# Kernel tuning notes

Hardware: AMD Instinct MI355X
Metric: run time of the kernel (lower is better)

## Reference

```python
import jax, jax.numpy as jnp
import numpy as np

NUM_NODES = 100000
FEAT_DIM = 256
H1 = 256
H2 = 256
NUM_CLASSES = 64
B = 4096
F1 = 25
F2 = 10


def setup_inputs() -> dict:
    key = jax.random.key(0)
    k0, k1, k2, ke, kw1, kw2, kw3 = jax.random.split(key, 7)
    T0 = jax.random.randint(k0, (B,), 0, NUM_NODES)
    T1 = jax.random.randint(k1, (B, F1), 0, NUM_NODES)
    T2 = jax.random.randint(k2, (B * F1, F2), 0, NUM_NODES)
    emb = jax.random.normal(ke, (NUM_NODES, FEAT_DIM), dtype=jnp.float32)
    # nn.Linear(in, out, bias=False) stores weight as [out, in]
    W1 = jax.random.normal(kw1, (H1, 2 * FEAT_DIM), dtype=jnp.float32) * (1.0 / np.sqrt(2 * FEAT_DIM))
    W2 = jax.random.normal(kw2, (H2, 2 * H1), dtype=jnp.float32) * (1.0 / np.sqrt(2 * H1))
    W3 = jax.random.normal(kw3, (NUM_CLASSES, H2), dtype=jnp.float32) * (1.0 / np.sqrt(H2))
    return {"T0": T0, "T1": T1, "T2": T2, "emb": emb, "W1": W1, "W2": W2, "W3": W3}


def reference(T0, T1, T2, emb, W1, W2, W3):
    # hop-0 roots: [B, D]; hop-1 neighbor mean: [B, D]
    feat_0 = emb[T0]
    x = emb[T1].mean(axis=1)
    h0 = jax.nn.relu(jnp.concatenate([feat_0, x], axis=1) @ W1.T)  # [B, H1]
    # dropout is identity in eval mode (p applied only in training)
    # hop-1 nodes with hop-2 neighbor mean: [B*F1, D] each
    feat_1 = emb[T1].reshape(-1, FEAT_DIM)
    x2 = emb[T2].mean(axis=1)  # [B*F1, D]
    h1 = jax.nn.relu(jnp.concatenate([feat_1, x2], axis=1) @ W1.T)  # [B*F1, H1]
    h1 = h1.reshape(B, F1, H1).mean(axis=1)  # [B, H1]
    combined = jnp.concatenate([h0, h1], axis=1)  # [B, 2*H1]
    embedding = jax.nn.relu(combined @ W2.T)  # [B, H2]
    scores = embedding @ W3.T  # [B, C]
    return scores
```

## Files before the change

kernel.cpp:

```cpp
#include <hip/hip_runtime.h>
#include <hip/hip_bf16.h>


typedef __bf16  bf16x8 __attribute__((ext_vector_type(8)));
typedef __bf16  bf16x4 __attribute__((ext_vector_type(4)));
typedef float   f32x4  __attribute__((ext_vector_type(4)));
typedef float   f32x2  __attribute__((ext_vector_type(2)));

#define BATCH     4096
#define F1        25
#define F2        10
#define NNODES    100000
#define ZY_NT     3125
#define ZY_BLOCKS 512

__device__ __forceinline__ uint2 pack4_bf16(float a, float b, float c, float d) {
    union { __bf16 h[4]; uint2 u; } p;
    p.h[0] = (__bf16)a; p.h[1] = (__bf16)b; p.h[2] = (__bf16)c; p.h[3] = (__bf16)d;
    return p.u;
}

__device__ __forceinline__ f32x2 pkmax0(f32x2 v) {
    f32x2 r; r[0] = fmaxf(v[0], 0.f); r[1] = fmaxf(v[1], 0.f); return r;
}

__global__ __launch_bounds__(256) void prep_weights(const float* __restrict__ W1,
                                                    const float* __restrict__ W2,
                                                    const float* __restrict__ W3,
                                                    __bf16* __restrict__ Wzy,
                                                    __bf16* __restrict__ W2b,
                                                    __bf16* __restrict__ W3b) {
    int blk = blockIdx.x;
    if (blk < 64) {
        int i = blk * 256 + threadIdx.x;
        int r  = i >> 5;
        int c0 = (i & 31) * 8;
        const float* src = (r < 256) ? (W1 + (size_t)r * 512 + c0)
                                     : (W1 + (size_t)(r - 256) * 512 + 256 + c0);
        float4 a = reinterpret_cast<const float4*>(src)[0];
        float4 b = reinterpret_cast<const float4*>(src)[1];
        uint4 o;
        uint2 pa = pack4_bf16(a.x, a.y, a.z, a.w);
        uint2 pb = pack4_bf16(b.x, b.y, b.z, b.w);
        o.x = pa.x; o.y = pa.y; o.z = pb.x; o.w = pb.y;
        *reinterpret_cast<uint4*>(Wzy + (size_t)r * 256 + c0) = o;
    } else {
        const float* in; __bf16* out;
        int i;
        if (blk < 128) { in = W2; out = W2b; i = (blk - 64) * 256 + threadIdx.x; }
        else           { in = W3; out = W3b; i = (blk - 128) * 256 + threadIdx.x; }
        float4 v0 = reinterpret_cast<const float4*>(in)[i * 2];
        float4 v1 = reinterpret_cast<const float4*>(in)[i * 2 + 1];
        uint4 o;
        uint2 a = pack4_bf16(v0.x, v0.y, v0.z, v0.w);
        uint2 b = pack4_bf16(v1.x, v1.y, v1.z, v1.w);
        o.x = a.x; o.y = a.y; o.z = b.x; o.w = b.y;
        reinterpret_cast<uint4*>(out)[i] = o;
    }
}

__global__ __launch_bounds__(512, 2) void gemm_ZY(const float* __restrict__ emb,
                                                  const __bf16* __restrict__ Wzy,
                                                  __bf16* __restrict__ Ztab,
                                                  unsigned char* __restrict__ Y8) {
    __shared__ __align__(16) char Abuf[2][16384];
    __shared__ __align__(16) __bf16 Ybuf[8][32][72];
    const int tid  = threadIdx.x;
    const int wid  = tid >> 6;
    const int lane = tid & 63;
    const int lr   = lane & 15;
    const int kg   = lane >> 4;
    const int n0   = wid * 64;

    bf16x8 wfrag[4][8];
    {
        const __bf16* Wb = Wzy + (size_t)(n0 + lr) * 256 + kg * 8;
#pragma unroll
        for (int ni = 0; ni < 4; ++ni)
#pragma unroll
            for (int kt = 0; kt < 8; ++kt)
                wfrag[ni][kt] = *reinterpret_cast<const bf16x8*>(Wb + ni * 16 * 256 + kt * 32);
    }

    int soff[4];
#pragma unroll
    for (int q = 0; q < 4; ++q) {
        int e  = q * 2048 + tid * 4;
        int r  = e >> 8;
        int cb = (e & 255) * 2;
        soff[q] = r * 512 + (cb ^ ((r & 7) << 4));
    }

    int t = blockIdx.x;
    float4 ld0[4];
    {
        const float4* src = reinterpret_cast<const float4*>(emb + (size_t)t * 8192);
#pragma unroll
        for (int q = 0; q < 4; ++q) ld0[q] = src[q * 512 + tid];
    }
    int cur = 0;

    for (; t < ZY_NT; t += ZY_BLOCKS) {
        int tn = t + ZY_BLOCKS;
        float4 ld1[4] = {};
        if (tn < ZY_NT) {
            const float4* src = reinterpret_cast<const float4*>(emb + (size_t)tn * 8192);
#pragma unroll
            for (int q = 0; q < 4; ++q) ld1[q] = src[q * 512 + tid];
        }
#pragma unroll
        for (int q = 0; q < 4; ++q) {
            float4 v = ld0[q];
            *reinterpret_cast<uint2*>(Abuf[cur] + soff[q]) = pack4_bf16(v.x, v.y, v.z, v.w);
        }
        asm volatile("s_waitcnt lgkmcnt(0)" ::: "memory");
        __builtin_amdgcn_s_barrier();

        f32x4 acc[2][4] = {};
        const char* Ab = Abuf[cur];
#pragma unroll
        for (int kt = 0; kt < 8; ++kt) {
            bf16x8 a[2];
#pragma unroll
            for (int mi = 0; mi < 2; ++mi) {
                int r  = mi * 16 + lr;
                int by = kt * 64 + kg * 16;
                a[mi] = *reinterpret_cast<const bf16x8*>(Ab + r * 512 + (by ^ ((r & 7) << 4)));
            }
#pragma unroll
            for (int mi = 0; mi < 2; ++mi)
#pragma unroll
                for (int ni = 0; ni < 4; ++ni)
                    acc[mi][ni] = __builtin_amdgcn_mfma_f32_16x16x32_bf16(a[mi], wfrag[ni][kt], acc[mi][ni], 0, 0, 0);
        }

        const int orow = (lane >> 4) * 4;
        const int ocol = lane & 15;
        const int m0   = t * 32;
#pragma unroll
        for (int mi = 0; mi < 2; ++mi)
#pragma unroll
            for (int ni = 0; ni < 4; ++ni)
#pragma unroll
                for (int j = 0; j < 4; ++j)
                    Ybuf[wid][mi * 16 + orow + j][ni * 16 + ocol] = (__bf16)acc[mi][ni][j];
        const int row = lane & 31;
        const int cg  = (lane >> 5) * 32;
        if (wid < 4) {
#pragma unroll
            for (int q = 0; q < 4; ++q) {
                bf16x8 v = *reinterpret_cast<bf16x8*>(&Ybuf[wid][row][cg + q * 8]);
                *reinterpret_cast<bf16x8*>(Ztab + (size_t)(m0 + row) * 256 + n0 + cg + q * 8) = v;
            }
        } else {
#pragma unroll
            for (int q = 0; q < 4; ++q) {
                bf16x8 v = *reinterpret_cast<bf16x8*>(&Ybuf[wid][row][cg + q * 8]);
                int w0 = 0, w1 = 0;
                w0 = __builtin_amdgcn_cvt_pk_fp8_f32((float)v[0], (float)v[1], w0, false);
                w0 = __builtin_amdgcn_cvt_pk_fp8_f32((float)v[2], (float)v[3], w0, true);
                w1 = __builtin_amdgcn_cvt_pk_fp8_f32((float)v[4], (float)v[5], w1, false);
                w1 = __builtin_amdgcn_cvt_pk_fp8_f32((float)v[6], (float)v[7], w1, true);
                uint2 o; o.x = (unsigned)w0; o.y = (unsigned)w1;
                *reinterpret_cast<uint2*>(Y8 + (size_t)(m0 + row) * 256 + (n0 - 256) + cg + q * 8) = o;
            }
        }

#pragma unroll
        for (int q = 0; q < 4; ++q) ld0[q] = ld1[q];
        cur ^= 1;
    }
}

__global__ __launch_bounds__(256) void agg_kernel(const int* __restrict__ T0,
                                                  const int* __restrict__ T1,
                                                  const int* __restrict__ T2,
                                                  const __bf16* __restrict__ Ztab,
                                                  const unsigned char* __restrict__ Y8,
                                                  __bf16* __restrict__ comb) {
    __shared__ float red1[4][256];
    __shared__ float red0[4][256];
    const int b    = blockIdx.x;
    const int wv   = threadIdx.x >> 6;
    const int lane = threadIdx.x & 63;

    f32x2 m01 = {0.f, 0.f}, m23 = {0.f, 0.f};
    f32x2 g01 = {0.f, 0.f}, g23 = {0.f, 0.f};

    int f = wv;
    int r0  = __builtin_amdgcn_readfirstlane(b * F1 + f);
    int t1c = T1[r0];
    bf16x4   zc  = *reinterpret_cast<const bf16x4*>(Ztab + (size_t)t1c * 256 + lane * 4);
    unsigned y1c = *reinterpret_cast<const unsigned*>(Y8 + (size_t)t1c * 256 + lane * 4);
    unsigned yvc[F2];
#pragma unroll
    for (int j = 0; j < F2; ++j) {
        int ix = T2[(size_t)r0 * F2 + j];
        yvc[j] = *reinterpret_cast<const unsigned*>(Y8 + (size_t)ix * 256 + lane * 4);
    }

    while (true) {
        const int fn = f + 4;
        const bool more = (fn < F1);
        bf16x4 zn; unsigned y1n; unsigned yvn[F2];
        if (more) {
            int rn  = __builtin_amdgcn_readfirstlane(b * F1 + fn);
            int t1n = T1[rn];
            zn  = *reinterpret_cast<const bf16x4*>(Ztab + (size_t)t1n * 256 + lane * 4);
            y1n = *reinterpret_cast<const unsigned*>(Y8 + (size_t)t1n * 256 + lane * 4);
#pragma unroll
            for (int j = 0; j < F2; ++j) {
                int ix = T2[(size_t)rn * F2 + j];
                yvn[j] = *reinterpret_cast<const unsigned*>(Y8 + (size_t)ix * 256 + lane * 4);
            }
        }
        f32x2 s01 = {0.f, 0.f}, s23 = {0.f, 0.f};
#pragma unroll
        for (int j = 0; j < F2; ++j) {
            s01 += __builtin_amdgcn_cvt_pk_f32_fp8(yvc[j], false);
            s23 += __builtin_amdgcn_cvt_pk_f32_fp8(yvc[j], true);
        }
        g01 += __builtin_amdgcn_cvt_pk_f32_fp8(y1c, false);
        g23 += __builtin_amdgcn_cvt_pk_f32_fp8(y1c, true);
        f32x2 z01; z01[0] = (float)zc[0]; z01[1] = (float)zc[1];
        f32x2 z23; z23[0] = (float)zc[2]; z23[1] = (float)zc[3];
        m01 += pkmax0(z01 + s01 * (1.0f / F2));
        m23 += pkmax0(z23 + s23 * (1.0f / F2));
        if (!more) break;
        f = fn; zc = zn; y1c = y1n;
#pragma unroll
        for (int j = 0; j < F2; ++j) yvc[j] = yvn[j];
    }

    {
        float4 t1v; t1v.x = m01[0]; t1v.y = m01[1]; t1v.z = m23[0]; t1v.w = m23[1];
        float4 t0v; t0v.x = g01[0]; t0v.y = g01[1]; t0v.z = g23[0]; t0v.w = g23[1];
        *reinterpret_cast<float4*>(&red1[wv][lane * 4]) = t1v;
        *reinterpret_cast<float4*>(&red0[wv][lane * 4]) = t0v;
    }
    __syncthreads();

    const int col = threadIdx.x;
    float s1 = red1[0][col] + red1[1][col] + red1[2][col] + red1[3][col];
    float s0 = red0[0][col] + red0[1][col] + red0[2][col] + red0[3][col];
    const int t0 = T0[b];
    float z0 = (float)Ztab[(size_t)t0 * 256 + col];
    comb[(size_t)b * 512 + col]       = (__bf16)fmaxf(z0 + s0 * (1.0f / F1), 0.0f);
    comb[(size_t)b * 512 + 256 + col] = (__bf16)(s1 * (1.0f / F1));
}

__global__ __launch_bounds__(256) void gemm_relu_bf16(const __bf16* __restrict__ A,
                                                      const __bf16* __restrict__ W,
                                                      __bf16* __restrict__ C,
                                                      int K, int ldc) {
    int wid  = threadIdx.x >> 6;
    int lane = threadIdx.x & 63;
    int m0 = blockIdx.x * 128 + (wid >> 1) * 64;
    int n0 = blockIdx.y * 128 + (wid & 1) * 64;
    int lr = lane & 15;
    int kg = lane >> 4;

    f32x4 acc[4][4] = {};
    const __bf16* Abase = A + (size_t)(m0 + lr) * K + kg * 8;
    const __bf16* Wbase = W + (size_t)(n0 + lr) * K + kg * 8;

    for (int kt = 0; kt < K; kt += 32) {
        bf16x8 a[4], b[4];
#pragma unroll
        for (int i = 0; i < 4; ++i)
            a[i] = *reinterpret_cast<const bf16x8*>(Abase + (size_t)i * 16 * K + kt);
#pragma unroll
        for (int i = 0; i < 4; ++i)
            b[i] = *reinterpret_cast<const bf16x8*>(Wbase + (size_t)i * 16 * K + kt);
#pragma unroll
        for (int mi = 0; mi < 4; ++mi)
#pragma unroll
            for (int ni = 0; ni < 4; ++ni)
                acc[mi][ni] = __builtin_amdgcn_mfma_f32_16x16x32_bf16(a[mi], b[ni], acc[mi][ni], 0, 0, 0);
    }

    int orow = (lane >> 4) * 4;
    int ocol = lane & 15;
#pragma unroll
    for (int mi = 0; mi < 4; ++mi)
#pragma unroll
        for (int ni = 0; ni < 4; ++ni)
#pragma unroll
            for (int j = 0; j < 4; ++j) {
                float v = fmaxf(acc[mi][ni][j], 0.0f);
                C[(size_t)(m0 + mi * 16 + orow + j) * ldc + (n0 + ni * 16 + ocol)] = (__bf16)v;
            }
}

__global__ __launch_bounds__(256) void gemm_out(const __bf16* __restrict__ A,
                                                const __bf16* __restrict__ W,
                                                float* __restrict__ C) {
    const int K = 256;
    int wid  = threadIdx.x >> 6;
    int lane = threadIdx.x & 63;
    int m0 = blockIdx.x * 128 + wid * 32;
    int lr = lane & 15;
    int kg = lane >> 4;

    f32x4 acc[2][4] = {};
    const __bf16* Abase = A + (size_t)(m0 + lr) * K + kg * 8;
    const __bf16* Wbase = W + (size_t)lr * K + kg * 8;

    for (int kt = 0; kt < K; kt += 32) {
        bf16x8 a[2], b[4];
#pragma unroll
        for (int i = 0; i < 2; ++i)
            a[i] = *reinterpret_cast<const bf16x8*>(Abase + (size_t)i * 16 * K + kt);
#pragma unroll
        for (int i = 0; i < 4; ++i)
            b[i] = *reinterpret_cast<const bf16x8*>(Wbase + (size_t)i * 16 * K + kt);
#pragma unroll
        for (int mi = 0; mi < 2; ++mi)
#pragma unroll
            for (int ni = 0; ni < 4; ++ni)
                acc[mi][ni] = __builtin_amdgcn_mfma_f32_16x16x32_bf16(a[mi], b[ni], acc[mi][ni], 0, 0, 0);
    }

    int orow = (lane >> 4) * 4;
    int ocol = lane & 15;
#pragma unroll
    for (int mi = 0; mi < 2; ++mi)
#pragma unroll
        for (int ni = 0; ni < 4; ++ni)
#pragma unroll
            for (int j = 0; j < 4; ++j)
                C[(size_t)(m0 + mi * 16 + orow + j) * 64 + (ni * 16 + ocol)] = acc[mi][ni][j];
}

extern "C" void kernel_launch(void* const* d_in, const int* in_sizes, int n_in,
                              void* d_out, int out_size, void* d_ws, size_t ws_size,
                              hipStream_t stream) {
    const int*   T0  = (const int*)d_in[0];
    const int*   T1  = (const int*)d_in[1];
    const int*   T2  = (const int*)d_in[2];
    const float* emb = (const float*)d_in[3];
    const float* W1  = (const float*)d_in[4];
    const float* W2  = (const float*)d_in[5];
    const float* W3  = (const float*)d_in[6];
    float* out = (float*)d_out;

    char* ws = (char*)d_ws;
    __bf16*        Wzy  = (__bf16*)(ws);
    __bf16*        W2b  = (__bf16*)(ws + 262144);
    __bf16*        W3b  = (__bf16*)(ws + 524288);
    __bf16*        comb = (__bf16*)(ws + 557056);
    __bf16*        embd = (__bf16*)(ws + 4751360);
    __bf16*        Ztab = (__bf16*)(ws + 6848512);
    unsigned char* Y8   = (unsigned char*)(ws + 58048512);

    prep_weights<<<dim3(136), dim3(256), 0, stream>>>(W1, W2, W3, Wzy, W2b, W3b);

    gemm_ZY<<<dim3(ZY_BLOCKS), dim3(512), 0, stream>>>(emb, Wzy, Ztab, Y8);

    agg_kernel<<<dim3(BATCH), dim3(256), 0, stream>>>(T0, T1, T2, Ztab, Y8, comb);

    gemm_relu_bf16<<<dim3(BATCH / 128, 2), dim3(256), 0, stream>>>(comb, W2b, embd, 512, 256);
    gemm_out<<<dim3(BATCH / 128), dim3(256), 0, stream>>>(embd, W3b, out);
}
```

Before: 133.5 us.

## Load embedding tiles directly into MFMA registers and split N across block pairs

The Z/Y projection kernel stops staging fp32 embedding tiles through a swizzled, double-buffered LDS buffer. Each wave now loads its A fragments straight from global memory, converts them to bf16 in registers, and swaps the MFMA operand order so the transposed output can be packed into LDS with 8-byte writes. The 512-thread blocks become pairs of 256-thread blocks that each handle half the output columns for the same row chunk, and the fp8 Y stores are widened to 16 bytes. This removes the barriers and LDS round-trip, but every wave re-reads the same embedding rows through the caches and the explicit next-tile prefetch is gone.

```diff
diff --git a/kernel.cpp b/kernel.cpp
--- a/kernel.cpp
+++ b/kernel.cpp
@@ -12,7 +12,7 @@
 #define F2        10
 #define NNODES    100000
 #define ZY_NT     3125
-#define ZY_BLOCKS 512
+#define ZY_CHUNKS 512
 
 __device__ __forceinline__ uint2 pack4_bf16(float a, float b, float c, float d) {
     union { __bf16 h[4]; uint2 u; } p;
@@ -59,18 +59,19 @@
     }
 }
 
-__global__ __launch_bounds__(512, 2) void gemm_ZY(const float* __restrict__ emb,
-                                                  const __bf16* __restrict__ Wzy,
-                                                  __bf16* __restrict__ Ztab,
-                                                  unsigned char* __restrict__ Y8) {
-    __shared__ __align__(16) char Abuf[2][16384];
-    __shared__ __align__(16) __bf16 Ybuf[8][32][72];
-    const int tid  = threadIdx.x;
-    const int wid  = tid >> 6;
-    const int lane = tid & 63;
-    const int lr   = lane & 15;
-    const int kg   = lane >> 4;
-    const int n0   = wid * 64;
+__global__ __launch_bounds__(256) void gemm_ZY(const float* __restrict__ emb,
+                                               const __bf16* __restrict__ Wzy,
+                                               __bf16* __restrict__ Ztab,
+                                               unsigned char* __restrict__ Y8) {
+    __shared__ __align__(16) __bf16 Ybuf[4][32][72];
+    const int tid   = threadIdx.x;
+    const int wid   = tid >> 6;
+    const int lane  = tid & 63;
+    const int lr    = lane & 15;
+    const int kg    = lane >> 4;
+    const int slice = ((blockIdx.x & 1) << 2) | wid;
+    const int n0    = slice * 64;
+    const int chunk = blockIdx.x >> 1;
 
     bf16x8 wfrag[4][8];
     {
@@ -82,71 +83,40 @@
                 wfrag[ni][kt] = *reinterpret_cast<const bf16x8*>(Wb + ni * 16 * 256 + kt * 32);
     }
 
-    int soff[4];
-#pragma unroll
-    for (int q = 0; q < 4; ++q) {
-        int e  = q * 2048 + tid * 4;
-        int r  = e >> 8;
-        int cb = (e & 255) * 2;
-        soff[q] = r * 512 + (cb ^ ((r & 7) << 4));
-    }
-
-    int t = blockIdx.x;
-    float4 ld0[4];
-    {
-        const float4* src = reinterpret_cast<const float4*>(emb + (size_t)t * 8192);
-#pragma unroll
-        for (int q = 0; q < 4; ++q) ld0[q] = src[q * 512 + tid];
-    }
-    int cur = 0;
-
-    for (; t < ZY_NT; t += ZY_BLOCKS) {
-        int tn = t + ZY_BLOCKS;
-        float4 ld1[4] = {};
-        if (tn < ZY_NT) {
-            const float4* src = reinterpret_cast<const float4*>(emb + (size_t)tn * 8192);
-#pragma unroll
-            for (int q = 0; q < 4; ++q) ld1[q] = src[q * 512 + tid];
+    for (int t = chunk; t < ZY_NT; t += ZY_CHUNKS) {
+        const int m0 = t * 32;
+        f32x4 acc[2][4] = {};
+        const float* Abase = emb + (size_t)(m0 + lr) * 256 + kg * 8;
+
+#pragma unroll 2
+        for (int kt = 0; kt < 8; ++kt) {
+#pragma unroll
+            for (int mi = 0; mi < 2; ++mi) {
+                const float* ap = Abase + (size_t)mi * 16 * 256 + kt * 32;
+                float4 f0 = reinterpret_cast<const float4*>(ap)[0];
+                float4 f1 = reinterpret_cast<const float4*>(ap)[1];
+                uint2 u0 = pack4_bf16(f0.x, f0.y, f0.z, f0.w);
+                uint2 u1 = pack4_bf16(f1.x, f1.y, f1.z, f1.w);
+                union { uint4 u; bf16x8 h; } a;
+                a.u.x = u0.x; a.u.y = u0.y; a.u.z = u1.x; a.u.w = u1.y;
+#pragma unroll
+                for (int ni = 0; ni < 4; ++ni)
+                    acc[mi][ni] = __builtin_amdgcn_mfma_f32_16x16x32_bf16(wfrag[ni][kt], a.h, acc[mi][ni], 0, 0, 0);
+            }
         }
-#pragma unroll
-        for (int q = 0; q < 4; ++q) {
-            float4 v = ld0[q];
-            *reinterpret_cast<uint2*>(Abuf[cur] + soff[q]) = pack4_bf16(v.x, v.y, v.z, v.w);
-        }
-        asm volatile("s_waitcnt lgkmcnt(0)" ::: "memory");
-        __builtin_amdgcn_s_barrier();
-
-        f32x4 acc[2][4] = {};
-        const char* Ab = Abuf[cur];
-#pragma unroll
-        for (int kt = 0; kt < 8; ++kt) {
-            bf16x8 a[2];
-#pragma unroll
-            for (int mi = 0; mi < 2; ++mi) {
-                int r  = mi * 16 + lr;
-                int by = kt * 64 + kg * 16;
-                a[mi] = *reinterpret_cast<const bf16x8*>(Ab + r * 512 + (by ^ ((r & 7) << 4)));
-            }
-#pragma unroll
-            for (int mi = 0; mi < 2; ++mi)
-#pragma unroll
-                for (int ni = 0; ni < 4; ++ni)
-                    acc[mi][ni] = __builtin_amdgcn_mfma_f32_16x16x32_bf16(a[mi], wfrag[ni][kt], acc[mi][ni], 0, 0, 0);
-        }
-
-        const int orow = (lane >> 4) * 4;
-        const int ocol = lane & 15;
-        const int m0   = t * 32;
+
+        const int csub = (lane >> 4) * 4;
 #pragma unroll
         for (int mi = 0; mi < 2; ++mi)
 #pragma unroll
-            for (int ni = 0; ni < 4; ++ni)
-#pragma unroll
-                for (int j = 0; j < 4; ++j)
-                    Ybuf[wid][mi * 16 + orow + j][ni * 16 + ocol] = (__bf16)acc[mi][ni][j];
+            for (int ni = 0; ni < 4; ++ni) {
+                f32x4 v = acc[mi][ni];
+                *reinterpret_cast<uint2*>(&Ybuf[wid][mi * 16 + lr][ni * 16 + csub]) =
+                    pack4_bf16(v[0], v[1], v[2], v[3]);
+            }
         const int row = lane & 31;
         const int cg  = (lane >> 5) * 32;
-        if (wid < 4) {
+        if (slice < 4) {
 #pragma unroll
             for (int q = 0; q < 4; ++q) {
                 bf16x8 v = *reinterpret_cast<bf16x8*>(&Ybuf[wid][row][cg + q * 8]);
@@ -154,21 +124,22 @@
             }
         } else {
 #pragma unroll
-            for (int q = 0; q < 4; ++q) {
-                bf16x8 v = *reinterpret_cast<bf16x8*>(&Ybuf[wid][row][cg + q * 8]);
-                int w0 = 0, w1 = 0;
-                w0 = __builtin_amdgcn_cvt_pk_fp8_f32((float)v[0], (float)v[1], w0, false);
-                w0 = __builtin_amdgcn_cvt_pk_fp8_f32((float)v[2], (float)v[3], w0, true);
-                w1 = __builtin_amdgcn_cvt_pk_fp8_f32((float)v[4], (float)v[5], w1, false);
-                w1 = __builtin_amdgcn_cvt_pk_fp8_f32((float)v[6], (float)v[7], w1, true);
-                uint2 o; o.x = (unsigned)w0; o.y = (unsigned)w1;
-                *reinterpret_cast<uint2*>(Y8 + (size_t)(m0 + row) * 256 + (n0 - 256) + cg + q * 8) = o;
+            for (int q = 0; q < 4; q += 2) {
+                bf16x8 v0 = *reinterpret_cast<bf16x8*>(&Ybuf[wid][row][cg + q * 8]);
+                bf16x8 v1 = *reinterpret_cast<bf16x8*>(&Ybuf[wid][row][cg + q * 8 + 8]);
+                int w0 = 0, w1 = 0, w2 = 0, w3 = 0;
+                w0 = __builtin_amdgcn_cvt_pk_fp8_f32((float)v0[0], (float)v0[1], w0, false);
+                w0 = __builtin_amdgcn_cvt_pk_fp8_f32((float)v0[2], (float)v0[3], w0, true);
+                w1 = __builtin_amdgcn_cvt_pk_fp8_f32((float)v0[4], (float)v0[5], w1, false);
+                w1 = __builtin_amdgcn_cvt_pk_fp8_f32((float)v0[6], (float)v0[7], w1, true);
+                w2 = __builtin_amdgcn_cvt_pk_fp8_f32((float)v1[0], (float)v1[1], w2, false);
+                w2 = __builtin_amdgcn_cvt_pk_fp8_f32((float)v1[2], (float)v1[3], w2, true);
+                w3 = __builtin_amdgcn_cvt_pk_fp8_f32((float)v1[4], (float)v1[5], w3, false);
+                w3 = __builtin_amdgcn_cvt_pk_fp8_f32((float)v1[6], (float)v1[7], w3, true);
+                uint4 o; o.x = (unsigned)w0; o.y = (unsigned)w1; o.z = (unsigned)w2; o.w = (unsigned)w3;
+                *reinterpret_cast<uint4*>(Y8 + (size_t)(m0 + row) * 256 + (n0 - 256) + cg + q * 8) = o;
             }
         }
-
-#pragma unroll
-        for (int q = 0; q < 4; ++q) ld0[q] = ld1[q];
-        cur ^= 1;
     }
 }
 
@@ -355,7 +326,7 @@
 
     prep_weights<<<dim3(136), dim3(256), 0, stream>>>(W1, W2, W3, Wzy, W2b, W3b);
 
-    gemm_ZY<<<dim3(ZY_BLOCKS), dim3(512), 0, stream>>>(emb, Wzy, Ztab, Y8);
+    gemm_ZY<<<dim3(1024), dim3(256), 0, stream>>>(emb, Wzy, Ztab, Y8);
 
     agg_kernel<<<dim3(BATCH), dim3(256), 0, stream>>>(T0, T1, T2, Ztab, Y8, comb);
 
```

After: 358.3 us. 168% more time.
